# Kernel optimization log

Hardware: AMD Instinct MI355X
Metric: run time of the kernel (lower is better)

The kernel has to match this reference:

```python
import jax, jax.numpy as jnp
import numpy as np

B, S, H = 2, 2048, 4096
NH, NKV, HD = 32, 8, 128
EPS = 1e-6


def _rope_tables(seq_len, head_dim, base=10000.0):
    inv = 1.0 / (base ** (np.arange(0, head_dim, 2, dtype=np.float32) / head_dim))
    t = np.arange(seq_len, dtype=np.float32)
    freqs = np.outer(t, inv)                       # [S, HD/2]
    emb = np.concatenate([freqs, freqs], axis=-1)  # [S, HD] (HF rotate_half layout)
    return jnp.asarray(np.cos(emb)), jnp.asarray(np.sin(emb))


def setup_inputs() -> dict:
    key = jax.random.key(0)
    ks = jax.random.split(key, 6)
    x = jax.random.normal(ks[0], (B, S, H), dtype=jnp.float32)
    wq = jax.random.normal(ks[1], (NH * HD, H), dtype=jnp.float32) * 0.02
    wk = jax.random.normal(ks[2], (NKV * HD, H), dtype=jnp.float32) * 0.02
    wv = jax.random.normal(ks[3], (NKV * HD, H), dtype=jnp.float32) * 0.02
    wo = jax.random.normal(ks[4], (H, NH * HD), dtype=jnp.float32) * 0.02
    cos1, sin1 = _rope_tables(S, HD)
    cos = jnp.broadcast_to(cos1[None], (B, S, HD))
    sin = jnp.broadcast_to(sin1[None], (B, S, HD))
    return {
        "x": x, "cos": cos, "sin": sin,
        "wq": wq, "wk": wk, "wv": wv, "wo": wo,
        "q_norm_w": jnp.ones((HD,), jnp.float32),
        "k_norm_w": jnp.ones((HD,), jnp.float32),
    }


def _rms_norm(x, w):
    # fp32 RMSNorm over last dim, scaled by per-head-dim weight
    xf = x.astype(jnp.float32)
    n = xf * jax.lax.rsqrt(jnp.mean(xf * xf, axis=-1, keepdims=True) + EPS)
    return n.astype(x.dtype) * w


def _rotate_half(x):
    x1, x2 = jnp.split(x, 2, axis=-1)
    return jnp.concatenate([-x2, x1], axis=-1)


def reference(x, cos, sin, wq, wk, wv, wo, q_norm_w, k_norm_w):
    bs, seqlen, _ = x.shape
    # projections (nn.Linear: y = x @ W^T)
    xq = (x @ wq.T).reshape(bs, seqlen, NH, HD)
    xk = (x @ wk.T).reshape(bs, seqlen, NKV, HD)
    xv = (x @ wv.T).reshape(bs, seqlen, NKV, HD)
    # per-head RMSNorm before RoPE
    xq = _rms_norm(xq, q_norm_w)
    xk = _rms_norm(xk, k_norm_w)
    # [b, h, s, d]
    xq = xq.transpose(0, 2, 1, 3)
    xk = xk.transpose(0, 2, 1, 3)
    xv = xv.transpose(0, 2, 1, 3)
    # RoPE, cos/sin broadcast over heads
    c = cos[:, None, :, :]
    s = sin[:, None, :, :]
    xq = xq * c + _rotate_half(xq) * s
    xk = xk * c + _rotate_half(xk) * s
    # GQA: repeat kv heads
    rep = NH // NKV
    if rep > 1:
        xk = jnp.repeat(xk, rep, axis=1)
        xv = jnp.repeat(xv, rep, axis=1)
    # causal SDPA
    scale = 1.0 / jnp.sqrt(jnp.float32(HD))
    scores = jnp.einsum("bhqd,bhkd->bhqk", xq, xk) * scale
    mask = jnp.tril(jnp.ones((seqlen, seqlen), bool))
    scores = jnp.where(mask, scores, jnp.finfo(scores.dtype).min)
    probs = jax.nn.softmax(scores, axis=-1)
    out = jnp.einsum("bhqk,bhkd->bhqd", probs, xv)
    out = out.transpose(0, 2, 1, 3).reshape(bs, seqlen, NH * HD)
    return out @ wo.T
```

## Files before the change

kernel.cpp:

```cpp
#include <hip/hip_runtime.h>
#include <hip/hip_bf16.h>

#define NB  2
#define SS  2048
#define HH  4096
#define NH  32
#define NKV 8
#define HD  128
#define MR  (NB*SS)

typedef __bf16 bf16x8 __attribute__((ext_vector_type(8)));
typedef float  f32x4  __attribute__((ext_vector_type(4)));
typedef float  f32x16 __attribute__((ext_vector_type(16)));
using bf16 = __hip_bfloat16;

__device__ __forceinline__ f32x4 mfma16(bf16x8 a, bf16x8 b, f32x4 c) {
  return __builtin_amdgcn_mfma_f32_16x16x32_bf16(a, b, c, 0, 0, 0);
}
__device__ __forceinline__ f32x16 mfma32(bf16x8 a, bf16x8 b, f32x16 c) {
  return __builtin_amdgcn_mfma_f32_32x32x16_bf16(a, b, c, 0, 0, 0);
}
__device__ __forceinline__ unsigned cvtpk(float lo, float hi) {
  unsigned r; asm("v_cvt_pk_bf16_f32 %0, %1, %2" : "=v"(r) : "v"(lo), "v"(hi));
  return r;
}
__device__ __forceinline__ void swap32(unsigned &a, unsigned &b) {
  asm volatile("v_permlane32_swap_b32 %0, %1" : "+v"(a), "+v"(b));
}
__device__ __forceinline__ float fexp2(float x) {
  float r; asm("v_exp_f32 %0, %1" : "=v"(r) : "v"(x)); return r;
}

typedef const __attribute__((address_space(1))) void gv_t;
typedef __attribute__((address_space(3))) void lv_t;
__device__ __forceinline__ void gload16(const void* g, void* l) {
  __builtin_amdgcn_global_load_lds((gv_t*)g, (lv_t*)l, 16, 0, 0);
}
#define CFENCE asm volatile("" ::: "memory")

__global__ void f2b5(const float* __restrict__ s0, const float* __restrict__ s1,
                     const float* __restrict__ s2, const float* __restrict__ s3,
                     const float* __restrict__ s4,
                     bf16* __restrict__ d0, bf16* __restrict__ d1,
                     bf16* __restrict__ d2, bf16* __restrict__ d3,
                     bf16* __restrict__ d4)
{
  const unsigned c0 = 4194304u, c1 = 8388608u, c2 = 9437184u, c3 = 10485760u,
                 c4 = 14680064u;
  unsigned i = blockIdx.x*blockDim.x + threadIdx.x;
  unsigned stride = gridDim.x*blockDim.x;
  for (unsigned u = i; u < c4; u += stride) {
    const float* s; bf16* d; unsigned off;
    if (u < c0)      { s = s0; d = d0; off = u; }
    else if (u < c1) { s = s1; d = d1; off = u - c0; }
    else if (u < c2) { s = s2; d = d2; off = u - c1; }
    else if (u < c3) { s = s3; d = d3; off = u - c2; }
    else             { s = s4; d = d4; off = u - c3; }
    float4 v = *(const float4*)(s + (size_t)off*4);
    __hip_bfloat16 b0 = __float2bfloat16(v.x);
    __hip_bfloat16 b1 = __float2bfloat16(v.y);
    __hip_bfloat16 b2 = __float2bfloat16(v.z);
    __hip_bfloat16 b3 = __float2bfloat16(v.w);
    ushort4 o;
    o.x = *reinterpret_cast<unsigned short*>(&b0);
    o.y = *reinterpret_cast<unsigned short*>(&b1);
    o.z = *reinterpret_cast<unsigned short*>(&b2);
    o.w = *reinterpret_cast<unsigned short*>(&b3);
    *(ushort4*)((unsigned short*)d + (size_t)off*4) = o;
  }
}

template<typename OutT>
__global__ __launch_bounds__(512, 2) void gemm256(
    const bf16* __restrict__ A, const bf16* __restrict__ Bt, OutT* __restrict__ C,
    int M, int N, int K, int tilesX)
{
  __shared__ bf16 lds[2*2*2*8192];

  const int bid = blockIdx.x;
  const int cpx = gridDim.x >> 3;
  const int wg  = (bid & 7)*cpx + (bid >> 3);
  const int m0 = (wg / tilesX) * 256, n0 = (wg % tilesX) * 256;

  const int tid = threadIdx.x;
  const int l = tid & 63;
  const int l15 = l & 15, lhi = l >> 4;
  const int wid = tid >> 6;
  const int wr = wid >> 2, wc = wid & 3;

  const int srow = tid >> 2;
  const int sps  = tid & 3;
  const int sls  = (sps - (srow >> 1)) & 3;
  const bf16* ga0 = A  + (size_t)(m0 + srow)*K       + sls*8;
  const bf16* ga1 = A  + (size_t)(m0 + srow + 128)*K + sls*8;
  const bf16* gb0 = Bt + (size_t)(n0 + srow)*K       + sls*8;
  const bf16* gb1 = Bt + (size_t)(n0 + srow + 128)*K + sls*8;
  const int ldst = tid*8;

#define REG(buf, mat, ks) (&lds[(((buf)*2 + (mat))*2 + (ks))*8192])
#define STG_A(buf, ks, kofs) do {                                 \
    gload16(ga0 + (kofs), REG(buf,0,ks) + ldst);                  \
    gload16(ga1 + (kofs), REG(buf,0,ks) + ldst + 4096);           \
  } while (0)
#define STG_B(buf, ks, kofs) do {                                 \
    gload16(gb0 + (kofs), REG(buf,1,ks) + ldst);                  \
    gload16(gb1 + (kofs), REG(buf,1,ks) + ldst + 4096);           \
  } while (0)

  f32x4 acc[8][4];
  #pragma unroll
  for (int fm = 0; fm < 8; ++fm)
    #pragma unroll
    for (int fn = 0; fn < 4; ++fn)
      #pragma unroll
      for (int e = 0; e < 4; ++e) acc[fm][fn][e] = 0.f;

  const int arow = wr*128 + l15;
  const int brow = wc*64  + l15;
  const int psl  = (lhi + (l15 >> 1)) & 3;

  bf16x8 bv[4];

#define PHASE(PB, KS, FMH, RB, STG, WN) do {                               \
    const bf16* Ar_ = REG(PB, 0, KS);                                      \
    const bf16* Br_ = REG(PB, 1, KS);                                      \
    bf16x8 af[4];                                                          \
    for (int fm = 0; fm < 4; ++fm)                                         \
      af[fm] = *(const bf16x8*)(Ar_ + (arow + (FMH)*64 + fm*16)*32 + psl*8); \
    if (RB) {                                                              \
      for (int fn = 0; fn < 4; ++fn)                                       \
        bv[fn] = *(const bf16x8*)(Br_ + (brow + fn*16)*32 + psl*8);        \
    }                                                                      \
    STG;                                                                   \
    CFENCE;                                                                \
    __builtin_amdgcn_s_barrier();                                          \
    __builtin_amdgcn_s_setprio(1);                                         \
    for (int fm = 0; fm < 4; ++fm)                                         \
      for (int fn = 0; fn < 4; ++fn)                                       \
        acc[(FMH)*4 + fm][fn] = mfma16(af[fm], bv[fn], acc[(FMH)*4 + fm][fn]); \
    __builtin_amdgcn_s_setprio(0);                                         \
    if ((WN) == 6)      asm volatile("s_waitcnt vmcnt(6)" ::: "memory");   \
    else if ((WN) == 0) asm volatile("s_waitcnt vmcnt(0)" ::: "memory");   \
    __builtin_amdgcn_s_barrier();                                          \
    CFENCE;                                                                \
  } while (0)

  const int nt = K >> 6;

  STG_A(0, 0, 0);  STG_B(0, 0, 0);  STG_A(0, 1, 32);  STG_B(0, 1, 32);
  STG_A(1, 0, 64); STG_B(1, 0, 64); STG_B(1, 1, 96);
  asm volatile("s_waitcnt vmcnt(6)" ::: "memory");
  __builtin_amdgcn_s_barrier();
  CFENCE;

  for (int i = 0; i < (nt >> 1) - 1; ++i) {
    const int t  = i << 1;
    const int k1 = ((t + 1) << 6) + 32;
    const int k2 = (t + 2) << 6;
    const int k3 = (t + 3) << 6;
    PHASE(0, 0, 0, true,  STG_A(1, 1, k1),      -1);
    PHASE(0, 0, 1, false, STG_B(0, 0, k2),      -1);
    PHASE(0, 1, 0, true,  STG_A(0, 0, k2),      -1);
    PHASE(0, 1, 1, false, STG_B(0, 1, k2 + 32),  6);
    PHASE(1, 0, 0, true,  STG_A(0, 1, k2 + 32), -1);
    PHASE(1, 0, 1, false, STG_B(1, 0, k3),      -1);
    PHASE(1, 1, 0, true,  STG_A(1, 0, k3),      -1);
    PHASE(1, 1, 1, false, STG_B(1, 1, k3 + 32),  6);
  }
  {
    const int k1 = ((nt - 1) << 6) + 32;
    PHASE(0, 0, 0, true,  STG_A(1, 1, k1), -1);
    PHASE(0, 0, 1, false, (void)0,         -1);
    PHASE(0, 1, 0, true,  (void)0,         -1);
    PHASE(0, 1, 1, false, (void)0,          0);
    PHASE(1, 0, 0, true,  (void)0,         -1);
    PHASE(1, 0, 1, false, (void)0,         -1);
    PHASE(1, 1, 0, true,  (void)0,         -1);
    PHASE(1, 1, 1, false, (void)0,         -1);
  }
#undef PHASE
#undef STG_A
#undef STG_B
#undef REG

  #pragma unroll
  for (int fm = 0; fm < 8; ++fm) {
    const int crow = m0 + wr*128 + fm*16 + lhi*4;
    #pragma unroll
    for (int fn = 0; fn < 4; ++fn) {
      const int ccol = n0 + wc*64 + fn*16 + l15;
      #pragma unroll
      for (int j = 0; j < 4; ++j) {
        if constexpr (sizeof(OutT) == 2)
          C[(size_t)(crow + j)*N + ccol] = __float2bfloat16(acc[fm][fn][j]);
        else
          C[(size_t)(crow + j)*N + ccol] = acc[fm][fn][j];
      }
    }
  }
}

__global__ __launch_bounds__(512, 2) void gemm128n(
    const bf16* __restrict__ A, const bf16* __restrict__ Bt, bf16* __restrict__ C,
    int M, int N, int K, int tilesX)
{
  __shared__ bf16 lds[2*2*12288];

  const int bid = blockIdx.x;
  const int cpx = gridDim.x >> 3;
  const int wg  = (bid & 7)*cpx + (bid >> 3);
  const int m0 = (wg / tilesX) * 128, n0 = (wg % tilesX) * 256;

  const int tid = threadIdx.x;
  const int l = tid & 63;
  const int l15 = l & 15, lhi = l >> 4;
  const int wid = tid >> 6;
  const int wr = wid >> 2, wc = wid & 3;

  const int srow = tid >> 2;
  const int sps  = tid & 3;
  const int sls  = (sps - (srow >> 1)) & 3;
  const bf16* gaA = A  + (size_t)(m0 + srow)*K       + sls*8;
  const bf16* gb0 = Bt + (size_t)(n0 + srow)*K       + sls*8;
  const bf16* gb1 = Bt + (size_t)(n0 + srow + 128)*K + sls*8;
  const int ldst = tid*8;

#define REGA(buf, ks) (&lds[((buf)*2 + (ks))*12288])
#define REGB(buf, ks) (&lds[((buf)*2 + (ks))*12288 + 4096])
#define STGKA(buf, ks, kofs) gload16(gaA + (kofs), REGA(buf,ks) + ldst)
#define STGKB(buf, ks, kofs) do {                                 \
    gload16(gb0 + (kofs), REGB(buf,ks) + ldst);                   \
    gload16(gb1 + (kofs), REGB(buf,ks) + ldst + 4096);            \
  } while (0)

  f32x4 acc[4][4];
  #pragma unroll
  for (int fm = 0; fm < 4; ++fm)
    #pragma unroll
    for (int fn = 0; fn < 4; ++fn)
      #pragma unroll
      for (int e = 0; e < 4; ++e) acc[fm][fn][e] = 0.f;

  const int arow = wr*64 + l15;
  const int brow = wc*64 + l15;
  const int psl  = (lhi + (l15 >> 1)) & 3;

#define PHASEK(PB, KS, STG, WN) do {                                       \
    const bf16* Ar_ = REGA(PB, KS);                                        \
    const bf16* Br_ = REGB(PB, KS);                                        \
    bf16x8 af[4], bv[4];                                                   \
    for (int fm = 0; fm < 4; ++fm)                                         \
      af[fm] = *(const bf16x8*)(Ar_ + (arow + fm*16)*32 + psl*8);          \
    for (int fn = 0; fn < 4; ++fn)                                         \
      bv[fn] = *(const bf16x8*)(Br_ + (brow + fn*16)*32 + psl*8);          \
    STG;                                                                   \
    CFENCE;                                                                \
    __builtin_amdgcn_s_barrier();                                          \
    __builtin_amdgcn_s_setprio(1);                                         \
    for (int fm = 0; fm < 4; ++fm)                                         \
      for (int fn = 0; fn < 4; ++fn)                                       \
        acc[fm][fn] = mfma16(af[fm], bv[fn], acc[fm][fn]);                 \
    __builtin_amdgcn_s_setprio(0);                                         \
    if ((WN) == 6)      asm volatile("s_waitcnt vmcnt(6)" ::: "memory");   \
    else if ((WN) == 0) asm volatile("s_waitcnt vmcnt(0)" ::: "memory");   \
    __builtin_amdgcn_s_barrier();                                          \
    CFENCE;                                                                \
  } while (0)

  const int nt = K >> 6;

  STGKB(0, 0, 0);  STGKA(0, 0, 0);  STGKB(0, 1, 32);  STGKA(0, 1, 32);
  STGKB(1, 0, 64); STGKA(1, 0, 64); STGKB(1, 1, 96);  STGKA(1, 1, 96);
  asm volatile("s_waitcnt vmcnt(6)" ::: "memory");
  __builtin_amdgcn_s_barrier();
  CFENCE;

  for (int i = 0; i < (nt >> 1) - 1; ++i) {
    const int t  = i << 1;
    const int k2 = (t + 2) << 6;
    const int k3 = (t + 3) << 6;
    PHASEK(0, 0, { STGKB(0, 0, k2);      STGKA(0, 0, k2);      }, -1);
    PHASEK(0, 1, { STGKB(0, 1, k2 + 32); STGKA(0, 1, k2 + 32); },  6);
    PHASEK(1, 0, { STGKB(1, 0, k3);      STGKA(1, 0, k3);      }, -1);
    PHASEK(1, 1, { STGKB(1, 1, k3 + 32); STGKA(1, 1, k3 + 32); },  6);
  }
  {
    PHASEK(0, 0, (void)0, -1);
    PHASEK(0, 1, (void)0,  0);
    PHASEK(1, 0, (void)0, -1);
    PHASEK(1, 1, (void)0, -1);
  }
#undef PHASEK
#undef STGKA
#undef STGKB
#undef REGA
#undef REGB

  #pragma unroll
  for (int fm = 0; fm < 4; ++fm) {
    const int crow = m0 + wr*64 + fm*16 + lhi*4;
    #pragma unroll
    for (int fn = 0; fn < 4; ++fn) {
      const int ccol = n0 + wc*64 + fn*16 + l15;
      #pragma unroll
      for (int j = 0; j < 4; ++j)
        C[(size_t)(crow + j)*N + ccol] = __float2bfloat16(acc[fm][fn][j]);
    }
  }
}

__global__ __launch_bounds__(256) void normrope2(
    const bf16* __restrict__ q0, const bf16* __restrict__ kv0,
    bf16* __restrict__ qr, bf16* __restrict__ kr,
    const float* __restrict__ cosb, const float* __restrict__ sinb,
    const float* __restrict__ qw_, const float* __restrict__ kw_)
{
  const unsigned QB = (MR*NH)/4;
  const int wid = threadIdx.x >> 6, lane = threadIdx.x & 63;
  const bf16* src; bf16* dst; const float* w; int nh, rowstride; float scale;
  int row;
  if (blockIdx.x < QB) {
    src = q0; dst = qr; w = qw_; nh = NH; rowstride = 4096;
    scale = 0.08838834764831845f*1.44269504088896341f;
    row = blockIdx.x*4 + wid;
  } else {
    src = kv0; dst = kr; w = kw_; nh = NKV; rowstride = 2048;
    scale = 1.0f;
    row = (blockIdx.x - QB)*4 + wid;
  }
  const int m = row / nh, h = row % nh;
  const int b = m / SS, s = m % SS;
  const bf16* sp = src + (size_t)m*rowstride + h*HD;
  float v1 = __bfloat162float(sp[lane]);
  float v2 = __bfloat162float(sp[lane + 64]);
  float ss = v1*v1 + v2*v2;
  #pragma unroll
  for (int msk = 1; msk < 64; msk <<= 1) ss += __shfl_xor(ss, msk);
  float r = rsqrtf(ss*(1.f/128.f) + 1e-6f) * scale;
  float n1 = v1*r*w[lane], n2 = v2*r*w[lane + 64];
  const float* cp  = cosb + (size_t)m*HD;
  const float* sip = sinb + (size_t)m*HD;
  float o1 = n1*cp[lane]      - n2*sip[lane];
  float o2 = n2*cp[lane + 64] + n1*sip[lane + 64];
  bf16* dp = dst + ((size_t)(b*nh + h)*SS + s)*HD;
  dp[lane]      = __float2bfloat16(o1);
  dp[lane + 64] = __float2bfloat16(o2);
}

__global__ __launch_bounds__(256) void vtrans(const bf16* __restrict__ v0,
                                              bf16* __restrict__ vt,
                                              int rowstride, int coloff)
{
  __shared__ bf16 tile[64][65];
  const int s0 = blockIdx.x*64, d0 = blockIdx.y*64, bkv = blockIdx.z;
  const int bb = bkv >> 3, kv = bkv & 7;
  const int c = threadIdx.x & 63, rbase = threadIdx.x >> 6;
  #pragma unroll
  for (int r = 0; r < 64; r += 4) {
    int sl = r + rbase;
    tile[sl][c] = v0[(size_t)(bb*SS + s0 + sl)*rowstride + coloff + kv*HD + d0 + c];
  }
  __syncthreads();
  #pragma unroll
  for (int r = 0; r < 64; r += 4) {
    int dl = r + rbase;
    vt[((size_t)bkv*HD + d0 + dl)*SS + s0 + c] = tile[c][dl];
  }
}

__global__ __launch_bounds__(512, 2) void attn_fwd(
    const bf16* __restrict__ qr, const bf16* __restrict__ kr,
    const bf16* __restrict__ vt, bf16* __restrict__ ao)
{
  __shared__ __align__(16) char smem[65536];

  const int L = blockIdx.x;
  const int j = L >> 6;
  const int bh = L & 63;
  const int b = bh >> 5, h = bh & 31, kvh = h >> 2;

  const int tid = threadIdx.x;
  const int wid = tid >> 6, lane = tid & 63;
  const int l31 = lane & 31, hi = lane >> 5;
  const unsigned hi16 = hi << 4;
  const unsigned swz = (lane & 7) << 4;

  const int qw0 = (wid < 4) ? (j*128 + wid*32) : ((15 - j)*128 + (wid - 4)*32);
  const int NT = 32 - 2*j;
  const int qlane = qw0 + l31;

  const bf16* Qp = qr + ((size_t)(b*NH + h)*SS + qlane)*HD;
  const bf16* Kp = kr + (size_t)(b*NKV + kvh)*SS*HD;
  const bf16* Vp = vt + (size_t)(b*NKV + kvh)*HD*SS;

  const int krA = tid >> 4;
  const int ksA = tid & 15;
  const int vrA = tid >> 3;
  const int vsA = tid & 7;
  const int kswz = (ksA ^ (krA & 7))*8;
  const int vswz = (vsA ^ (vrA & 7))*8;

#define STAGE_ATTN(buf, kvbase) do {                                        \
    char* kb = smem + (buf)*32768;                                          \
    char* vb = kb + 16384;                                                  \
    gload16(Kp + (size_t)(krA + (kvbase))*HD + kswz,      kb + tid*16);     \
    gload16(Kp + (size_t)(krA + 32 + (kvbase))*HD + kswz, kb + 8192 + tid*16); \
    gload16(Vp + (size_t)vrA*SS + (kvbase) + vswz,        vb + tid*16);     \
    gload16(Vp + (size_t)(vrA + 64)*SS + (kvbase) + vswz, vb + 8192 + tid*16); \
  } while (0)

  STAGE_ATTN(0, 0);
  bf16x8 qf[8];
  #pragma unroll
  for (int kd = 0; kd < 8; ++kd)
    qf[kd] = *(const bf16x8*)(Qp + kd*16 + hi*8);
  asm volatile("s_waitcnt vmcnt(0)" ::: "memory");
  __builtin_amdgcn_s_barrier();
  CFENCE;

  f32x16 o0, o1, o2, o3;
  #pragma unroll
  for (int r = 0; r < 16; ++r) { o0[r] = 0.f; o1[r] = 0.f; o2[r] = 0.f; o3[r] = 0.f; }
  float mrow = -1e30f, lrow = 0.f;

  for (int t = 0; t < NT; ++t) {
    const int p = t & 1;
    const char* KsB = smem + p*32768;
    const char* VsB = KsB + 16384;
    if (t + 1 < NT) STAGE_ATTN(p ^ 1, (t + 1)*64);
    const int kv0 = t*64;

    if (kv0 <= qw0 + 31) {
      f32x16 s0, s1;
      #pragma unroll
      for (int r = 0; r < 16; ++r) { s0[r] = 0.f; s1[r] = 0.f; }
      #pragma unroll
      for (int kd = 0; kd < 8; ++kd) {
        bf16x8 k0f = *(const bf16x8*)(KsB + l31*256        + (((unsigned)(kd*32) + hi16) ^ swz));
        bf16x8 k1f = *(const bf16x8*)(KsB + (32 + l31)*256 + (((unsigned)(kd*32) + hi16) ^ swz));
        s0 = mfma32(k0f, qf[kd], s0);
        s1 = mfma32(k1f, qf[kd], s1);
      }
      if (kv0 + 63 > qw0) {
        #pragma unroll
        for (int r = 0; r < 16; ++r) {
          const int off = (r & 3) + 8*(r >> 2) + 4*hi;
          if (kv0 + off > qlane)      s0[r] = -1e30f;
          if (kv0 + 32 + off > qlane) s1[r] = -1e30f;
        }
      }
      float mg[8];
      #pragma unroll
      for (int r = 0; r < 8; ++r)
        mg[r] = fmaxf(fmaxf(s0[r], s0[r + 8]), fmaxf(s1[r], s1[r + 8]));
      float ta = fmaxf(fmaxf(mg[0], mg[1]), mg[2]);
      float tb = fmaxf(fmaxf(mg[3], mg[4]), mg[5]);
      float tmax = fmaxf(fmaxf(ta, tb), fmaxf(mg[6], mg[7]));
      tmax = fmaxf(tmax, __shfl_xor(tmax, 32));
      if (!__all(tmax <= mrow + 8.f)) {
        float mnew = fmaxf(mrow, tmax);
        float alpha = fexp2(mrow - mnew);
        mrow = mnew;
        lrow *= alpha;
        #pragma unroll
        for (int r = 0; r < 16; ++r) {
          o0[r] *= alpha; o1[r] *= alpha; o2[r] *= alpha; o3[r] *= alpha;
        }
      }
      float tsum = 0.f;
      #pragma unroll
      for (int r = 0; r < 16; ++r) { s0[r] = fexp2(s0[r] - mrow); tsum += s0[r]; }
      #pragma unroll
      for (int r = 0; r < 16; ++r) { s1[r] = fexp2(s1[r] - mrow); tsum += s1[r]; }
      tsum += __shfl_xor(tsum, 32);
      lrow += tsum;

      #pragma unroll
      for (int ks = 0; ks < 4; ++ks) {
        const int bb0 = (ks & 1)*8;
        float p0,p1,p2,p3,p4,p5,p6,p7;
        if (ks < 2) { p0=s0[bb0+0];p1=s0[bb0+1];p2=s0[bb0+2];p3=s0[bb0+3];
                      p4=s0[bb0+4];p5=s0[bb0+5];p6=s0[bb0+6];p7=s0[bb0+7]; }
        else        { p0=s1[bb0+0];p1=s1[bb0+1];p2=s1[bb0+2];p3=s1[bb0+3];
                      p4=s1[bb0+4];p5=s1[bb0+5];p6=s1[bb0+6];p7=s1[bb0+7]; }
        unsigned c01 = cvtpk(p0,p1), c23 = cvtpk(p2,p3);
        unsigned c45 = cvtpk(p4,p5), c67 = cvtpk(p6,p7);
        unsigned w0 = c01, w2 = c45; swap32(w0, w2);
        unsigned w1 = c23, w3 = c67; swap32(w1, w3);
        union { unsigned u[4]; bf16x8 v; } pa;
        pa.u[0]=w0; pa.u[1]=w1; pa.u[2]=w2; pa.u[3]=w3;
        #pragma unroll
        for (int dt = 0; dt < 4; ++dt) {
          bf16x8 vf = *(const bf16x8*)(VsB + (dt*32 + l31)*128 +
                                       (((unsigned)(ks*32) + hi16) ^ swz));
          f32x16 &oo = (dt==0)?o0:(dt==1)?o1:(dt==2)?o2:o3;
          oo = mfma32(vf, pa.v, oo);
        }
      }
    }

    asm volatile("s_waitcnt vmcnt(0)" ::: "memory");
    __builtin_amdgcn_s_barrier();
    CFENCE;
  }
#undef STAGE_ATTN

  const float invl = 1.f / lrow;
  char* ow = smem + wid*4096;
  bf16* aop = ao + ((size_t)b*SS + qlane)*HH + h*HD;
  const unsigned eswz = (l31 & 7) << 4;
  #pragma unroll
  for (int half = 0; half < 2; ++half) {
    #pragma unroll
    for (int hh = 0; hh < 2; ++hh) {
      #pragma unroll
      for (int r = 0; r < 16; ++r) {
        const int dcol = hh*32 + (r & 3) + 8*(r >> 2) + 4*hi;
        float val = ((half*2+hh)==0 ? o0[r] : (half*2+hh)==1 ? o1[r]
                     : (half*2+hh)==2 ? o2[r] : o3[r]) * invl;
        *(bf16*)(ow + l31*128 + (((unsigned)(dcol*2)) ^ eswz)) = __float2bfloat16(val);
      }
    }
    #pragma unroll
    for (int m = 0; m < 4; ++m) {
      const int c0 = hi*32 + m*8;
      bf16x8 vv = *(const bf16x8*)(ow + l31*128 + (((unsigned)(c0*2)) ^ eswz));
      *(bf16x8*)(aop + half*64 + c0) = vv;
    }
  }
}

extern "C" void kernel_launch(void* const* d_in, const int* in_sizes, int n_in,
                              void* d_out, int out_size, void* d_ws, size_t ws_size,
                              hipStream_t stream)
{
  const float* x    = (const float*)d_in[0];
  const float* cosb = (const float*)d_in[1];
  const float* sinb = (const float*)d_in[2];
  const float* wq   = (const float*)d_in[3];
  const float* wk   = (const float*)d_in[4];
  const float* wv   = (const float*)d_in[5];
  const float* wo   = (const float*)d_in[6];
  const float* qnw  = (const float*)d_in[7];
  const float* knw  = (const float*)d_in[8];
  float* out = (float*)d_out;

  char* ws = (char*)d_ws;
  bf16* xb    = (bf16*)(ws);
  bf16* wqkvb = (bf16*)(ws +  33554432);
  bf16* wob   = (bf16*)(ws +  83886080);
  bf16* q0    = (bf16*)(ws + 117440512);
  bf16* kv0   = (bf16*)(ws + 150994944);
  bf16* qr    = (bf16*)(ws + 167772160);
  bf16* vt = xb;
  bf16* kr = (bf16*)(ws + 8388608);
  bf16* ao = q0;

  f2b5<<<2048, 256, 0, stream>>>(x, wq, wk, wv, wo,
                                 xb, wqkvb,
                                 wqkvb + (size_t)4096*4096,
                                 wqkvb + (size_t)5120*4096,
                                 wob);

  gemm256<bf16><<<256, 512, 0, stream>>>(xb, wqkvb, q0, MR, 4096, HH, 16);
  gemm128n<<<256, 512, 0, stream>>>(xb, wqkvb + (size_t)4096*4096, kv0,
                                    MR, 2048, HH, 8);

  normrope2<<<(MR*NH)/4 + (MR*NKV)/4, 256, 0, stream>>>(
      q0, kv0, qr, kr, cosb, sinb, qnw, knw);
  vtrans<<<dim3(32, 2, 16), 256, 0, stream>>>(kv0, vt, 2048, 1024);

  attn_fwd<<<512, 512, 0, stream>>>(qr, kr, vt, ao);

  gemm256<float><<<256, 512, 0, stream>>>(ao, wob, out, MR, HH, HH, 16);
}
```

Baseline: 500.1 us.

## Merge Q and KV projection GEMMs and fuse V transpose with norm-RoPE kernel

Combines the Q projection GEMM and the KV projection GEMM into a single launch that branches on block index, so the 256+256 workgroups can run concurrently rather than back to back. Folds the V transpose into the norm/RoPE postprocessing kernel for the same reason. Moves the cross-half row-sum shuffle in attention out of the inner loop to a single reduction at the end. This removes launch gaps and tail underutilisation. The cost is a larger shared-memory footprint for the fused GEMM and more divergent kernel bodies.

```diff
diff --git a/kernel.cpp b/kernel.cpp
--- a/kernel.cpp
+++ b/kernel.cpp
@@ -71,14 +71,11 @@
 }
 
 template<typename OutT>
-__global__ __launch_bounds__(512, 2) void gemm256(
-    const bf16* __restrict__ A, const bf16* __restrict__ Bt, OutT* __restrict__ C,
-    int M, int N, int K, int tilesX)
-{
-  __shared__ bf16 lds[2*2*2*8192];
-
-  const int bid = blockIdx.x;
-  const int cpx = gridDim.x >> 3;
+__device__ __forceinline__ void gemm256_body(
+    bf16* lds, const bf16* __restrict__ A, const bf16* __restrict__ Bt,
+    OutT* __restrict__ C, int bid, int N, int K, int tilesX)
+{
+  const int cpx = 32;
   const int wg  = (bid & 7)*cpx + (bid >> 3);
   const int m0 = (wg / tilesX) * 256, n0 = (wg % tilesX) * 256;
 
@@ -200,14 +197,11 @@
   }
 }
 
-__global__ __launch_bounds__(512, 2) void gemm128n(
-    const bf16* __restrict__ A, const bf16* __restrict__ Bt, bf16* __restrict__ C,
-    int M, int N, int K, int tilesX)
-{
-  __shared__ bf16 lds[2*2*12288];
-
-  const int bid = blockIdx.x;
-  const int cpx = gridDim.x >> 3;
+__device__ __forceinline__ void gemm128n_body(
+    bf16* lds, const bf16* __restrict__ A, const bf16* __restrict__ Bt,
+    bf16* __restrict__ C, int bid, int N, int K, int tilesX)
+{
+  const int cpx = 32;
   const int wg  = (bid & 7)*cpx + (bid >> 3);
   const int m0 = (wg / tilesX) * 128, n0 = (wg % tilesX) * 256;
 
@@ -309,24 +303,65 @@
   }
 }
 
-__global__ __launch_bounds__(256) void normrope2(
+__global__ __launch_bounds__(512, 2) void qkvproj(
+    const bf16* __restrict__ xb, const bf16* __restrict__ wqkvb,
+    bf16* __restrict__ q0, bf16* __restrict__ kv0)
+{
+  __shared__ bf16 lds[2*2*2*8192];
+  if (blockIdx.x < 256)
+    gemm256_body<bf16>(lds, xb, wqkvb, q0, blockIdx.x, 4096, HH, 16);
+  else
+    gemm128n_body(lds, xb, wqkvb + (size_t)4096*4096, kv0,
+                  blockIdx.x - 256, 2048, HH, 8);
+}
+
+__global__ __launch_bounds__(512, 2) void oproj(
+    const bf16* __restrict__ ao, const bf16* __restrict__ wob,
+    float* __restrict__ out)
+{
+  __shared__ bf16 lds[2*2*2*8192];
+  gemm256_body<float>(lds, ao, wob, out, blockIdx.x, HH, HH, 16);
+}
+
+__global__ __launch_bounds__(256) void postproc(
     const bf16* __restrict__ q0, const bf16* __restrict__ kv0,
-    bf16* __restrict__ qr, bf16* __restrict__ kr,
+    bf16* __restrict__ qr, bf16* __restrict__ kr, bf16* __restrict__ vt,
     const float* __restrict__ cosb, const float* __restrict__ sinb,
     const float* __restrict__ qw_, const float* __restrict__ kw_)
 {
+  __shared__ bf16 tile[64][65];
+  if (blockIdx.x < 1024) {
+    const int idx = blockIdx.x;
+    const int bkv = idx & 15, dby = (idx >> 4) & 1, sbx = idx >> 5;
+    const int s0 = sbx*64, d0 = dby*64;
+    const int bb = bkv >> 3, kv = bkv & 7;
+    const int c = threadIdx.x & 63, rbase = threadIdx.x >> 6;
+    #pragma unroll
+    for (int r = 0; r < 64; r += 4) {
+      int sl = r + rbase;
+      tile[sl][c] = kv0[(size_t)(bb*SS + s0 + sl)*2048 + 1024 + kv*HD + d0 + c];
+    }
+    __syncthreads();
+    #pragma unroll
+    for (int r = 0; r < 64; r += 4) {
+      int dl = r + rbase;
+      vt[((size_t)bkv*HD + d0 + dl)*SS + s0 + c] = tile[c][dl];
+    }
+    return;
+  }
+  const unsigned blk = blockIdx.x - 1024;
   const unsigned QB = (MR*NH)/4;
   const int wid = threadIdx.x >> 6, lane = threadIdx.x & 63;
   const bf16* src; bf16* dst; const float* w; int nh, rowstride; float scale;
   int row;
-  if (blockIdx.x < QB) {
+  if (blk < QB) {
     src = q0; dst = qr; w = qw_; nh = NH; rowstride = 4096;
     scale = 0.08838834764831845f*1.44269504088896341f;
-    row = blockIdx.x*4 + wid;
+    row = blk*4 + wid;
   } else {
     src = kv0; dst = kr; w = kw_; nh = NKV; rowstride = 2048;
     scale = 1.0f;
-    row = (blockIdx.x - QB)*4 + wid;
+    row = (blk - QB)*4 + wid;
   }
   const int m = row / nh, h = row % nh;
   const int b = m / SS, s = m % SS;
@@ -345,27 +380,6 @@
   bf16* dp = dst + ((size_t)(b*nh + h)*SS + s)*HD;
   dp[lane]      = __float2bfloat16(o1);
   dp[lane + 64] = __float2bfloat16(o2);
-}
-
-__global__ __launch_bounds__(256) void vtrans(const bf16* __restrict__ v0,
-                                              bf16* __restrict__ vt,
-                                              int rowstride, int coloff)
-{
-  __shared__ bf16 tile[64][65];
-  const int s0 = blockIdx.x*64, d0 = blockIdx.y*64, bkv = blockIdx.z;
-  const int bb = bkv >> 3, kv = bkv & 7;
-  const int c = threadIdx.x & 63, rbase = threadIdx.x >> 6;
-  #pragma unroll
-  for (int r = 0; r < 64; r += 4) {
-    int sl = r + rbase;
-    tile[sl][c] = v0[(size_t)(bb*SS + s0 + sl)*rowstride + coloff + kv*HD + d0 + c];
-  }
-  __syncthreads();
-  #pragma unroll
-  for (int r = 0; r < 64; r += 4) {
-    int dl = r + rbase;
-    vt[((size_t)bkv*HD + d0 + dl)*SS + s0 + c] = tile[c][dl];
-  }
 }
 
 __global__ __launch_bounds__(512, 2) void attn_fwd(
@@ -472,7 +486,6 @@
       for (int r = 0; r < 16; ++r) { s0[r] = fexp2(s0[r] - mrow); tsum += s0[r]; }
       #pragma unroll
       for (int r = 0; r < 16; ++r) { s1[r] = fexp2(s1[r] - mrow); tsum += s1[r]; }
-      tsum += __shfl_xor(tsum, 32);
       lrow += tsum;
 
       #pragma unroll
@@ -505,6 +518,8 @@
   }
 #undef STAGE_ATTN
 
+  lrow += __shfl_xor(lrow, 32);
+
   const float invl = 1.f / lrow;
   char* ow = smem + wid*4096;
   bf16* aop = ao + ((size_t)b*SS + qlane)*HH + h*HD;
@@ -562,15 +577,12 @@
                                  wqkvb + (size_t)5120*4096,
                                  wob);
 
-  gemm256<bf16><<<256, 512, 0, stream>>>(xb, wqkvb, q0, MR, 4096, HH, 16);
-  gemm128n<<<256, 512, 0, stream>>>(xb, wqkvb + (size_t)4096*4096, kv0,
-                                    MR, 2048, HH, 8);
-
-  normrope2<<<(MR*NH)/4 + (MR*NKV)/4, 256, 0, stream>>>(
-      q0, kv0, qr, kr, cosb, sinb, qnw, knw);
-  vtrans<<<dim3(32, 2, 16), 256, 0, stream>>>(kv0, vt, 2048, 1024);
+  qkvproj<<<512, 512, 0, stream>>>(xb, wqkvb, q0, kv0);
+
+  postproc<<<1024 + (MR*NH)/4 + (MR*NKV)/4, 256, 0, stream>>>(
+      q0, kv0, qr, kr, vt, cosb, sinb, qnw, knw);
 
   attn_fwd<<<512, 512, 0, stream>>>(qr, kr, vt, ao);
 
-  gemm256<float><<<256, 512, 0, stream>>>(ao, wob, out, MR, HH, HH, 16);
-}
+  oproj<<<256, 512, 0, stream>>>(ao, wob, out);
+}
```

Measured after the change: 491.6 us. Within noise of the previous version (-1.7%).
